# Optimization experiments

Measured on AMD Instinct MI355X. Metric: run time of the kernel, lower is better.

## Reference

```python
import jax, jax.numpy as jnp
import numpy as np
from jax import lax


def _lstm(x, W_ih, W_hh, b_ih, b_hh, return_seq):
    """PyTorch-compatible single-layer LSTM, batch_first, zero init state.
    W_ih: [4H, D], W_hh: [4H, H], gate order (i, f, g, o).
    Returns [B, T, H] if return_seq else final hidden [B, H]."""
    B, T, _ = x.shape
    H = W_hh.shape[1]
    # Precompute input contribution for all timesteps: [B, T, 4H]
    xg = jnp.einsum('btd,gd->btg', x, W_ih) + b_ih + b_hh
    h0 = jnp.zeros((B, H), x.dtype)
    c0 = jnp.zeros((B, H), x.dtype)

    def step(carry, xt):
        h, c = carry
        g = xt + h @ W_hh.T  # [B, 4H]
        i, f, gg, o = jnp.split(g, 4, axis=-1)
        i = jax.nn.sigmoid(i)
        f = jax.nn.sigmoid(f)
        gg = jnp.tanh(gg)
        o = jax.nn.sigmoid(o)
        c = f * c + i * gg
        h = o * jnp.tanh(c)
        return (h, c), (h if return_seq else None)

    (hT, _), ys = lax.scan(step, (h0, c0), jnp.swapaxes(xg, 0, 1))
    if return_seq:
        return jnp.swapaxes(ys, 0, 1)  # [B, T, H]
    return hT


def setup_inputs() -> dict:
    key = jax.random.key(0)
    ks = jax.random.split(key, 12)
    B, T, D = 2048, 512, 64
    H1, H2 = 16, 4
    s = 0.1
    return {
        'x': jax.random.normal(ks[0], (B, T, D), jnp.float32),
        'W_ih1': jax.random.normal(ks[1], (4 * H1, D), jnp.float32) * s,
        'W_hh1': jax.random.normal(ks[2], (4 * H1, H1), jnp.float32) * s,
        'b_ih1': jax.random.normal(ks[3], (4 * H1,), jnp.float32) * s,
        'b_hh1': jax.random.normal(ks[4], (4 * H1,), jnp.float32) * s,
        'W_ih2': jax.random.normal(ks[5], (4 * H2, H1), jnp.float32) * s,
        'W_hh2': jax.random.normal(ks[6], (4 * H2, H2), jnp.float32) * s,
        'b_ih2': jax.random.normal(ks[7], (4 * H2,), jnp.float32) * s,
        'b_hh2': jax.random.normal(ks[8], (4 * H2,), jnp.float32) * s,
        'W_fc': jax.random.normal(ks[9], (D, H2), jnp.float32) * s,
        'b_fc': jax.random.normal(ks[10], (D,), jnp.float32) * s,
    }


def reference(x, W_ih1, W_hh1, b_ih1, b_hh1, W_ih2, W_hh2, b_ih2, b_hh2, W_fc, b_fc):
    y = _lstm(x, W_ih1, W_hh1, b_ih1, b_hh1, return_seq=True)  # [B, T, H1]
    y = jax.nn.relu(y)
    # Only the last timestep of lstm2 is used -> return final hidden state.
    y_last = _lstm(y, W_ih2, W_hh2, b_ih2, b_hh2, return_seq=False)  # [B, H2]
    out = y_last @ W_fc.T + b_fc  # [B, D]
    return jax.nn.sigmoid(out)
```

## Files before the change

### kernel.cpp

```cpp
#include <hip/hip_runtime.h>
#include <hip/hip_bf16.h>

#define T_ALL 512
#define TB 16
#define NB (T_ALL / TB)
#define LOG2E 1.44269504088896f
#define XSTR 68

typedef __attribute__((ext_vector_type(8))) short bf16x8;
typedef __attribute__((ext_vector_type(4))) float f32x4;

#define DPPF(v, CTRL) __uint_as_float((unsigned)__builtin_amdgcn_update_dpp(0, (int)__float_as_uint(v), (CTRL), 0xF, 0xF, true))
#define SWZF(v, PAT)  __uint_as_float((unsigned)__builtin_amdgcn_ds_swizzle((int)__float_as_uint(v), (PAT)))
#define BPERM(a, v)   __uint_as_float((unsigned)__builtin_amdgcn_ds_bpermute((a), (int)__float_as_uint(v)))

__device__ __forceinline__ unsigned pack2fast(float a, float b) {
    const unsigned ua = __float_as_uint(a) + 0x8000u;
    const unsigned ub = __float_as_uint(b) + 0x8000u;
    return __builtin_amdgcn_perm(ub, ua, 0x07060302u);
}
__device__ __forceinline__ bf16x8 make_frag(float4 lo, float4 hi) {
    union { unsigned u[4]; bf16x8 v; } r;
    r.u[0] = pack2fast(lo.x, lo.y);
    r.u[1] = pack2fast(lo.z, lo.w);
    r.u[2] = pack2fast(hi.x, hi.y);
    r.u[3] = pack2fast(hi.z, hi.w);
    return r.v;
}
__device__ __forceinline__ float4 scale4(float4 v, float s) {
    return make_float4(v.x * s, v.y * s, v.z * s, v.w * s);
}
__device__ __forceinline__ float4 relu4(float4 v) {
    return make_float4(fmaxf(v.x, 0.f), fmaxf(v.y, 0.f), fmaxf(v.z, 0.f), fmaxf(v.w, 0.f));
}
__device__ __forceinline__ float2 pkfma(float2 a, float2 b, float2 c) {
    return make_float2(fmaf(a.x, b.x, c.x), fmaf(a.y, b.y, c.y));
}
__device__ __forceinline__ float2 pkmul(float2 a, float2 b) {
    return make_float2(a.x * b.x, a.y * b.y);
}
__device__ __forceinline__ float tanh_c(float c) {
    return fmaf(2.0f, __builtin_amdgcn_rcpf(
        1.0f + __builtin_amdgcn_exp2f(-2.0f * LOG2E * c)), -1.0f);
}
__device__ __forceinline__ float fsigm(float x) {
    return __builtin_amdgcn_rcpf(1.0f + __builtin_amdgcn_exp2f(-LOG2E * x));
}

__global__ __launch_bounds__(128, 4)
void lstm_fused_v9(const float* __restrict__ x,
        const float* __restrict__ Wih1, const float* __restrict__ Whh1,
        const float* __restrict__ bih1, const float* __restrict__ bhh1,
        const float* __restrict__ Wih2, const float* __restrict__ Whh2,
        const float* __restrict__ bih2, const float* __restrict__ bhh2,
        const float* __restrict__ Wfc,  const float* __restrict__ bfc,
        float* __restrict__ out)
{
    __shared__ __align__(16) float xgl[2][TB * XSTR];
    __shared__ __align__(16) float h1l[2][TB][16];
    __shared__ __align__(16) float xg2l[TB * 16];

    const int tid = threadIdx.x;
    const int wid = tid >> 6;
    const int lane = tid & 63;
    const size_t b = blockIdx.x;

    const int tl = lane & 15;
    const int kh = lane >> 4;
    const int T1 = lane & 3;
    const int j1 = lane >> 2;

    const float aA1 = (T1 == 2) ? 2.0f : 1.0f, aB1 = (T1 == 2) ? -1.0f : 0.0f;

    bf16x8 wb[4][2];
    float bias1[4];
#pragma unroll
    for (int n = 0; n < 4; ++n) {
        const float scn = (n == 2) ? 2.0f * LOG2E : LOG2E;
#pragma unroll
        for (int kk = 0; kk < 2; ++kk) {
            const float* wp = Wih1 + (size_t)(n * 16 + tl) * 64 + kk * 32 + kh * 8;
            wb[n][kk] = make_frag(scale4(*(const float4*)wp, scn),
                                  scale4(*(const float4*)(wp + 4), scn));
        }
        bias1[n] = (bih1[n * 16 + tl] + bhh1[n * 16 + tl]) * scn;
    }

    float2 wrA0, wrA1, wrB0, wrB1, wrC0, wrC1, wrD0, wrD1;
    {
        const float sA = (T1 == 2) ? 2.0f * LOG2E : LOG2E;
        const float sB = ((T1 ^ 2) == 2) ? 2.0f * LOG2E : LOG2E;
        const float sC = ((T1 ^ 1) == 2) ? 2.0f * LOG2E : LOG2E;
        const float sD = ((T1 ^ 3) == 2) ? 2.0f * LOG2E : LOG2E;
        const float4 wa  = scale4(*(const float4*)(Whh1 + ((T1    ) * 16 + j1) * 16 + 4 * T1), sA);
        const float4 wbv = scale4(*(const float4*)(Whh1 + ((T1 ^ 2) * 16 + j1) * 16 + 4 * T1), sB);
        const float4 wc  = scale4(*(const float4*)(Whh1 + ((T1 ^ 1) * 16 + j1) * 16 + 4 * T1), sC);
        const float4 wd  = scale4(*(const float4*)(Whh1 + ((T1 ^ 3) * 16 + j1) * 16 + 4 * T1), sD);
        wrA0 = make_float2(wa.x, wa.y);   wrA1 = make_float2(wa.z, wa.w);
        wrB0 = make_float2(wbv.x, wbv.y); wrB1 = make_float2(wbv.z, wbv.w);
        wrC0 = make_float2(wc.x, wc.y);   wrC1 = make_float2(wc.z, wc.w);
        wrD0 = make_float2(wd.x, wd.y);   wrD1 = make_float2(wd.z, wd.w);
    }

    bf16x8 wA2;
    {
        union { unsigned u[4]; bf16x8 v; } z;
        z.u[0] = z.u[1] = z.u[2] = z.u[3] = 0u;
        wA2 = z.v;
        if (kh < 2) {
            const float scr = ((tl >> 2) == 2) ? 2.0f * LOG2E : LOG2E;
            const float* wp = Wih2 + tl * 16 + kh * 8;
            wA2 = make_frag(scale4(*(const float4*)wp, scr),
                            scale4(*(const float4*)(wp + 4), scr));
        }
    }
    f32x4 bias2v;
#pragma unroll
    for (int r = 0; r < 4; ++r) {
        const int g = 4 * kh + r;
        bias2v[r] = (bih2[g] + bhh2[g]) * (((g >> 2) == 2) ? 2.0f * LOG2E : LOG2E);
    }

    const int m2 = lane >> 4;
    const int T2 = (lane >> 2) & 3;
    const int s2 = lane & 3;
    const int row2 = T2 * 4 + m2;
    const float sc2 = (T2 == 2) ? 2.0f * LOG2E : LOG2E;
    const float aA2 = (T2 == 2) ? 2.0f : 1.0f, aB2 = (T2 == 2) ? -1.0f : 0.0f;
    const float w2h = Whh2[row2 * 4 + s2] * sc2;
    const float4 wfc = *(const float4*)(Wfc + lane * 4);
    const float bfcv = bfc[lane];

    const int ag0 = (16 * T1 + 0)  << 2;
    const int ag1 = (16 * T1 + 4)  << 2;
    const int ag2 = (16 * T1 + 8)  << 2;
    const int ag3 = (16 * T1 + 12) << 2;
    const int ahs = s2 << 6;
    const int gidx = T1 * 16 + j1;

    float c1r = 0.f, h1r = 0.f;
    float c2r = 0.f, h2v = 0.f, h2s = 0.f;

    const float* xb = x + b * (size_t)(T_ALL * 64);
    float4 xpf[4];

#define LOADX(CH) do { \
    const float* _src = xb + (size_t)(CH) * (TB * 64); \
    _Pragma("unroll") \
    for (int _kk = 0; _kk < 2; ++_kk) \
        _Pragma("unroll") \
        for (int _hf = 0; _hf < 2; ++_hf) \
            xpf[_kk * 2 + _hf] = *(const float4*)(_src + tl * 64 + _kk * 32 + kh * 8 + _hf * 4); \
} while (0)

#define STEP1(XU) do { \
    const float _g0 = BPERM(ag0, h1r); \
    const float _g1 = BPERM(ag1, h1r); \
    const float _g2 = BPERM(ag2, h1r); \
    const float _g3 = BPERM(ag3, h1r); \
    const float2 _g01 = make_float2(_g0, _g1); \
    const float2 _g23 = make_float2(_g2, _g3); \
    float2 _aA = pkmul(wrA0, _g01); _aA = pkfma(wrA1, _g23, _aA); \
    float2 _aB = pkmul(wrB0, _g01); _aB = pkfma(wrB1, _g23, _aB); \
    float2 _aC = pkmul(wrC0, _g01); _aC = pkfma(wrC1, _g23, _aC); \
    float2 _aD = pkmul(wrD0, _g01); _aD = pkfma(wrD1, _g23, _aD); \
    const float _sA = _aA.x + _aA.y, _sB2 = _aB.x + _aB.y; \
    const float _sC = _aC.x + _aC.y, _sD = _aD.x + _aD.y; \
    const float _u0 = _sA + DPPF(_sC, 0xB1); \
    const float _u1 = _sB2 + DPPF(_sD, 0xB1); \
    const float _pre = _u0 + DPPF(_u1, 0x4E) + (XU); \
    const float _s1 = __builtin_amdgcn_rcpf(1.0f + __builtin_amdgcn_exp2f(-_pre)); \
    const float _act = fmaf(aA1, _s1, aB1); \
    const float _fv = DPPF(_act, 0x55); \
    const float _gv = DPPF(_act, 0xAA); \
    const float _ov = DPPF(_act, 0xFF); \
    c1r = fmaf(_fv, c1r, _act * _gv);         \
    h1r = _ov * tanh_c(c1r);                  \
} while (0)

#define GATES2(RG) do { \
    bf16x8 _bf; \
    { union { unsigned u[4]; bf16x8 v; } _z; _z.u[0]=_z.u[1]=_z.u[2]=_z.u[3]=0u; _bf = _z.v; } \
    if (kh < 2) { \
        const float4 _h0 = *(const float4*)&h1l[RG][tl][8 * kh]; \
        const float4 _h1 = *(const float4*)&h1l[RG][tl][8 * kh + 4]; \
        _bf = make_frag(relu4(_h0), relu4(_h1)); \
    } \
    f32x4 _acc = bias2v; \
    _acc = __builtin_amdgcn_mfma_f32_16x16x32_bf16(wA2, _bf, _acc, 0, 0, 0); \
    _Pragma("unroll") \
    for (int _r = 0; _r < 4; ++_r) \
        xg2l[tl * 16 + 4 * kh + _r] = _acc[_r]; \
} while (0)

#define LSTM2_STEP(TT) do { \
    const float _xg2 = xg2l[(TT) * 16 + row2]; \
    float _p2 = w2h * h2s; \
    _p2 += DPPF(_p2, 0xB1); \
    _p2 += DPPF(_p2, 0x4E); \
    _p2 += _xg2; \
    const float _act2 = fmaf(aA2, \
        __builtin_amdgcn_rcpf(1.0f + __builtin_amdgcn_exp2f(-_p2)), aB2); \
    const float _fv2 = SWZF(_act2, 0x101F); \
    const float _gv2 = SWZF(_act2, 0x201F); \
    const float _ov2 = SWZF(_act2, 0x301F); \
    c2r = fmaf(_fv2, c2r, _act2 * _gv2);      \
    h2v = _ov2 * tanh_c(c2r); \
    h2s = BPERM(ahs, h2v); \
} while (0)

    if (wid == 1) {
        LOADX(0);
        {
            bf16x8 a0s = make_frag(xpf[0], xpf[1]);
            bf16x8 a1s = make_frag(xpf[2], xpf[3]);
#pragma unroll
            for (int n = 0; n < 4; ++n) {
                f32x4 acc = {bias1[n], bias1[n], bias1[n], bias1[n]};
                acc = __builtin_amdgcn_mfma_f32_16x16x32_bf16(a0s, wb[n][0], acc, 0, 0, 0);
                acc = __builtin_amdgcn_mfma_f32_16x16x32_bf16(a1s, wb[n][1], acc, 0, 0, 0);
#pragma unroll
                for (int r = 0; r < 4; ++r)
                    xgl[0][(kh * 4 + r) * XSTR + n * 16 + tl] = acc[r];
            }
        }
        LOADX(1);
    }
    __syncthreads();

    for (int c = 0; c < NB; ++c) {
        if (wid == 0) {
            const float* xrow = &xgl[c & 1][0];
            const int rg = c & 1;
#pragma unroll
            for (int tt = 0; tt < TB; ++tt) {
                const float xu = xrow[tt * XSTR + gidx];
                STEP1(xu);
                if (T1 == 0) h1l[rg][tt][j1] = h1r;
            }
        } else {
            if (c + 1 < NB) {
                bf16x8 a0s = make_frag(xpf[0], xpf[1]);
                bf16x8 a1s = make_frag(xpf[2], xpf[3]);
                if (c + 2 < NB) LOADX(c + 2);
#pragma unroll
                for (int n = 0; n < 4; ++n) {
                    f32x4 acc = {bias1[n], bias1[n], bias1[n], bias1[n]};
                    acc = __builtin_amdgcn_mfma_f32_16x16x32_bf16(a0s, wb[n][0], acc, 0, 0, 0);
                    acc = __builtin_amdgcn_mfma_f32_16x16x32_bf16(a1s, wb[n][1], acc, 0, 0, 0);
#pragma unroll
                    for (int r = 0; r < 4; ++r)
                        xgl[(c + 1) & 1][(kh * 4 + r) * XSTR + n * 16 + tl] = acc[r];
                }
            }
            if (c >= 1) {
                GATES2((c - 1) & 1);
#pragma unroll
                for (int tt = 0; tt < TB; ++tt)
                    LSTM2_STEP(tt);
            }
        }
        __syncthreads();
    }

    if (wid == 1) {
        GATES2((NB - 1) & 1);
#pragma unroll
        for (int tt = 0; tt < TB; ++tt)
            LSTM2_STEP(tt);

        const float hq0 = __shfl(h2v, 0);
        const float hq1 = __shfl(h2v, 16);
        const float hq2 = __shfl(h2v, 32);
        const float hq3 = __shfl(h2v, 48);
        float accf = bfcv;
        accf = fmaf(wfc.x, hq0, accf);
        accf = fmaf(wfc.y, hq1, accf);
        accf = fmaf(wfc.z, hq2, accf);
        accf = fmaf(wfc.w, hq3, accf);
        out[b * 64 + lane] = fsigm(accf);
    }
#undef LOADX
#undef STEP1
#undef GATES2
#undef LSTM2_STEP
}

extern "C" void kernel_launch(void* const* d_in, const int* in_sizes, int n_in,
                              void* d_out, int out_size, void* d_ws, size_t ws_size,
                              hipStream_t stream) {
    const float* x    = (const float*)d_in[0];
    const float* Wih1 = (const float*)d_in[1];
    const float* Whh1 = (const float*)d_in[2];
    const float* bih1 = (const float*)d_in[3];
    const float* bhh1 = (const float*)d_in[4];
    const float* Wih2 = (const float*)d_in[5];
    const float* Whh2 = (const float*)d_in[6];
    const float* bih2 = (const float*)d_in[7];
    const float* bhh2 = (const float*)d_in[8];
    const float* Wfc  = (const float*)d_in[9];
    const float* bfc  = (const float*)d_in[10];
    float* out = (float*)d_out;

    lstm_fused_v9<<<dim3(2048), dim3(128), 0, stream>>>(
        x, Wih1, Whh1, bih1, bhh1, Wih2, Whh2, bih2, bhh2, Wfc, bfc, out);
}
```

Measured before the change: 161.7 us.

## Split LSTM2 onto a dedicated third wave and read h1 from LDS

The block grows from two to three waves. The second LSTM's per-chunk recurrence moves off the MFMA input-projection wave onto its own wave, so the projection and LSTM2 stages run concurrently with the layer-1 recurrence. The layer-1 step now loads the previous hidden vector as a float4 from the shared h1 buffer instead of four ds_bpermute broadcasts. This trades cross-lane permutes for an LDS store-to-load dependency, and raises thread count per block, which may lower register budget and occupancy.

```diff
diff --git a/kernel.cpp b/kernel.cpp
--- a/kernel.cpp
+++ b/kernel.cpp
@@ -47,8 +47,8 @@
     return __builtin_amdgcn_rcpf(1.0f + __builtin_amdgcn_exp2f(-LOG2E * x));
 }
 
-__global__ __launch_bounds__(128, 4)
-void lstm_fused_v9(const float* __restrict__ x,
+__global__ __launch_bounds__(192, 6)
+void lstm_fused_v10(const float* __restrict__ x,
         const float* __restrict__ Wih1, const float* __restrict__ Whh1,
         const float* __restrict__ bih1, const float* __restrict__ bhh1,
         const float* __restrict__ Wih2, const float* __restrict__ Whh2,
@@ -131,10 +131,6 @@
     const float4 wfc = *(const float4*)(Wfc + lane * 4);
     const float bfcv = bfc[lane];
 
-    const int ag0 = (16 * T1 + 0)  << 2;
-    const int ag1 = (16 * T1 + 4)  << 2;
-    const int ag2 = (16 * T1 + 8)  << 2;
-    const int ag3 = (16 * T1 + 12) << 2;
     const int ahs = s2 << 6;
     const int gidx = T1 * 16 + j1;
 
@@ -153,13 +149,24 @@
             xpf[_kk * 2 + _hf] = *(const float4*)(_src + tl * 64 + _kk * 32 + kh * 8 + _hf * 4); \
 } while (0)
 
-#define STEP1(XU) do { \
-    const float _g0 = BPERM(ag0, h1r); \
-    const float _g1 = BPERM(ag1, h1r); \
-    const float _g2 = BPERM(ag2, h1r); \
-    const float _g3 = BPERM(ag3, h1r); \
-    const float2 _g01 = make_float2(_g0, _g1); \
-    const float2 _g23 = make_float2(_g2, _g3); \
+#define MFMA_XG(BUF) do { \
+    bf16x8 _a0 = make_frag(xpf[0], xpf[1]); \
+    bf16x8 _a1 = make_frag(xpf[2], xpf[3]); \
+    _Pragma("unroll") \
+    for (int _n = 0; _n < 4; ++_n) { \
+        f32x4 _acc = {bias1[_n], bias1[_n], bias1[_n], bias1[_n]}; \
+        _acc = __builtin_amdgcn_mfma_f32_16x16x32_bf16(_a0, wb[_n][0], _acc, 0, 0, 0); \
+        _acc = __builtin_amdgcn_mfma_f32_16x16x32_bf16(_a1, wb[_n][1], _acc, 0, 0, 0); \
+        _Pragma("unroll") \
+        for (int _r = 0; _r < 4; ++_r) \
+            xgl[BUF][(kh * 4 + _r) * XSTR + _n * 16 + tl] = _acc[_r]; \
+    } \
+} while (0)
+
+#define STEP1(XU, HP) do { \
+    const float4 _gq = *(const float4*)((HP) + 4 * T1); \
+    const float2 _g01 = make_float2(_gq.x, _gq.y); \
+    const float2 _g23 = make_float2(_gq.z, _gq.w); \
     float2 _aA = pkmul(wrA0, _g01); _aA = pkfma(wrA1, _g23, _aA); \
     float2 _aB = pkmul(wrB0, _g01); _aB = pkfma(wrB1, _g23, _aB); \
     float2 _aC = pkmul(wrC0, _g01); _aC = pkfma(wrC1, _g23, _aC); \
@@ -209,34 +216,31 @@
     h2s = BPERM(ahs, h2v); \
 } while (0)
 
-    if (wid == 1) {
+    if (wid == 2) {
         LOADX(0);
-        {
-            bf16x8 a0s = make_frag(xpf[0], xpf[1]);
-            bf16x8 a1s = make_frag(xpf[2], xpf[3]);
-#pragma unroll
-            for (int n = 0; n < 4; ++n) {
-                f32x4 acc = {bias1[n], bias1[n], bias1[n], bias1[n]};
-                acc = __builtin_amdgcn_mfma_f32_16x16x32_bf16(a0s, wb[n][0], acc, 0, 0, 0);
-                acc = __builtin_amdgcn_mfma_f32_16x16x32_bf16(a1s, wb[n][1], acc, 0, 0, 0);
-#pragma unroll
-                for (int r = 0; r < 4; ++r)
-                    xgl[0][(kh * 4 + r) * XSTR + n * 16 + tl] = acc[r];
-            }
-        }
+        MFMA_XG(0);
         LOADX(1);
     }
+    if (wid == 0 && T1 == 0) h1l[1][15][j1] = 0.f;
     __syncthreads();
 
     for (int c = 0; c < NB; ++c) {
         if (wid == 0) {
             const float* xrow = &xgl[c & 1][0];
             const int rg = c & 1;
+            const float* hprev0 = &h1l[rg ^ 1][15][0];
 #pragma unroll
             for (int tt = 0; tt < TB; ++tt) {
-                const float xu = xrow[tt * XSTR + gidx];
-                STEP1(xu);
+                const float* hp = (tt == 0) ? hprev0 : &h1l[rg][tt - 1][0];
+                STEP1(xrow[tt * XSTR + gidx], hp);
                 if (T1 == 0) h1l[rg][tt][j1] = h1r;
+            }
+        } else if (wid == 1) {
+            if (c >= 1) {
+                GATES2((c - 1) & 1);
+#pragma unroll
+                for (int tt = 0; tt < TB; ++tt)
+                    LSTM2_STEP(tt);
             }
         } else {
             if (c + 1 < NB) {
@@ -252,12 +256,6 @@
                     for (int r = 0; r < 4; ++r)
                         xgl[(c + 1) & 1][(kh * 4 + r) * XSTR + n * 16 + tl] = acc[r];
                 }
-            }
-            if (c >= 1) {
-                GATES2((c - 1) & 1);
-#pragma unroll
-                for (int tt = 0; tt < TB; ++tt)
-                    LSTM2_STEP(tt);
             }
         }
         __syncthreads();
@@ -281,6 +279,7 @@
         out[b * 64 + lane] = fsigm(accf);
     }
 #undef LOADX
+#undef MFMA_XG
 #undef STEP1
 #undef GATES2
 #undef LSTM2_STEP
@@ -302,6 +301,6 @@
     const float* bfc  = (const float*)d_in[10];
     float* out = (float*)d_out;
 
-    lstm_fused_v9<<<dim3(2048), dim3(128), 0, stream>>>(
+    lstm_fused_v10<<<dim3(2048), dim3(192), 0, stream>>>(
         x, Wih1, Whh1, bih1, bhh1, Wih2, Whh2, bih2, bhh2, Wfc, bfc, out);
 }
```

Result: slower. 215.6 us (+33.3%).
